# Optimization experiments

Measured on AMD Instinct MI355X. Metric: run time of the kernel, lower is better.

The kernel has to match this reference:

```python
import jax, jax.numpy as jnp
import numpy as np

MARGIN = 1.0
NUM_CLASSES = 128


def setup_inputs() -> dict:
    key = jax.random.key(0)
    k1, k2, k3, k4, k5, k6 = jax.random.split(key, 6)
    B, D, C = 131072, 256, NUM_CLASSES
    return {
        "embeddings": jax.random.normal(k1, (B, D), dtype=jnp.float32),
        "labels": jax.random.randint(k2, (B,), 0, C),
        "W": jax.random.normal(k3, (C, D), dtype=jnp.float32),
        "b": jax.random.normal(k4, (C,), dtype=jnp.float32),
        "r_pos": jax.random.randint(k5, (B,), 0, 1000000007),
        "r_neg": jax.random.randint(k6, (B,), 0, 1000000007),
    }


def reference(embeddings, labels, W, b, r_pos, r_neg):
    B = embeddings.shape[0]
    C = W.shape[0]
    labels = labels.astype(jnp.int32)
    r_pos = r_pos.astype(jnp.int32)
    r_neg = r_neg.astype(jnp.int32)

    # ---- classifier under no_grad: argmax/top-2 of softmax == of logits ----
    logits = jax.lax.stop_gradient(embeddings) @ W.T + b  # [B, C]
    _, top2 = jax.lax.top_k(logits, 2)
    predicted = top2[:, 0]
    runner_up = top2[:, 1]
    correct = predicted == labels
    target_neg = jnp.where(correct, runner_up, predicted)  # [B]

    # ---- per-class segments: sort indices by label once ----
    counts = jnp.zeros((C,), jnp.int32).at[labels].add(1)      # [C]
    starts = jnp.cumsum(counts) - counts                       # [C] segment starts
    order = jnp.argsort(labels).astype(jnp.int32)              # [B] sorted-by-label index list
    inv = jnp.zeros((B,), jnp.int32).at[order].set(jnp.arange(B, dtype=jnp.int32))
    rank = inv - starts[labels]                                # anchor's position within its class segment

    # ---- vectorized masked random sampling ----
    n_pos = counts[labels] - 1                                 # positives exclude the anchor itself
    pr = r_pos % jnp.maximum(n_pos, 1)
    pr = pr + (pr >= rank).astype(jnp.int32)                   # skip over anchor's own slot
    pos_idx = order[starts[labels] + pr]

    n_neg = counts[target_neg]                                 # target_neg != label, anchor never in set
    nr = r_neg % jnp.maximum(n_neg, 1)
    neg_idx = order[starts[target_neg] + nr]

    # ---- triplet margin loss ----
    d_pos = jnp.linalg.norm(embeddings - embeddings[pos_idx], axis=1)
    d_neg = jnp.linalg.norm(embeddings - embeddings[neg_idx], axis=1)
    loss = jnp.maximum(d_pos - d_neg + MARGIN, 0.0)

    valid = (n_pos > 0) & (n_neg > 0)
    loss = loss * valid.astype(loss.dtype)
    denom = jnp.maximum(valid.sum(), 1).astype(loss.dtype)
    return loss.sum() / denom
```

## Files before the change

kernel.cpp:

```cpp
#include <hip/hip_runtime.h>
#include <cstdint>
#include <cstddef>

constexpr int D = 256;
constexpr int C = 128;
constexpr float MARGIN = 1.0f;

typedef __attribute__((ext_vector_type(8))) short short8;
typedef __attribute__((ext_vector_type(4))) float f32x4;

__device__ inline unsigned f2bf(float x) {
    unsigned u = __float_as_uint(x);
    return (u + 0x7FFFu + ((u >> 16) & 1u)) >> 16;
}

__device__ inline void cvt_split8(const float* xs, short8& h, short8& l) {
#pragma unroll
    for (int j = 0; j < 8; ++j) {
        float x = xs[j];
        unsigned hb = f2bf(x);
        h[j] = (short)hb;
        float hf = __uint_as_float(hb << 16);
        l[j] = (short)f2bf(x - hf);
    }
}

__device__ __forceinline__ void merge_top2(float& v1, int& i1, float& v2, int& i2,
                                           float w1, int j1, float w2, int j2)
{
    bool b = (w1 > v1) || (w1 == v1 && j1 < i1);
    float best_v = b ? w1 : v1; int best_i = b ? j1 : i1;
    float lose_v = b ? v1 : w1; int lose_i = b ? i1 : j1;
    float sec_v  = b ? w2 : v2; int sec_i  = b ? j2 : i2;
    bool c = (lose_v > sec_v) || (lose_v == sec_v && lose_i < sec_i);
    v1 = best_v; i1 = best_i;
    v2 = c ? lose_v : sec_v; i2 = c ? lose_i : sec_i;
}

__launch_bounds__(512, 4)
__global__ void k1_logits_top2(const float* __restrict__ emb,
                               const int*   __restrict__ labels,
                               const float* __restrict__ W,
                               const float* __restrict__ bias,
                               int*         __restrict__ target_neg,
                               unsigned short* __restrict__ embh,
                               int do_store)
{
    __shared__ char ldsW[C * 512];
    __shared__ float ldsBias[C];
    const int tid = threadIdx.x;

#pragma unroll
    for (int c = tid; c < 4096; c += 512) {
        int n = c >> 5, slot = c & 31;
        const float* src = W + n * 256 + slot * 8;
        float4 f0 = *(const float4*)src;
        float4 f1 = *(const float4*)(src + 4);
        short8 h;
        h[0] = (short)f2bf(f0.x); h[1] = (short)f2bf(f0.y);
        h[2] = (short)f2bf(f0.z); h[3] = (short)f2bf(f0.w);
        h[4] = (short)f2bf(f1.x); h[5] = (short)f2bf(f1.y);
        h[6] = (short)f2bf(f1.z); h[7] = (short)f2bf(f1.w);
        int dst = (n * 512 + slot * 16) ^ ((n & 7) << 4);
        *(short8*)(ldsW + dst) = h;
    }
    if (tid < C) ldsBias[tid] = bias[tid];
    __syncthreads();

    const int wid = tid >> 6, lane = tid & 63;
    const int l15 = lane & 15, lq = lane >> 4;
    const long row0 = (long)blockIdx.x * 256 + wid * 32;

    f32x4 acc[2][8];
#pragma unroll
    for (int rt = 0; rt < 2; ++rt)
#pragma unroll
        for (int t = 0; t < 8; ++t) acc[rt][t] = (f32x4){0.f, 0.f, 0.f, 0.f};

    const float* e0 = emb + (size_t)(row0 + l15) * D + 8 * lq;
    const float* e1 = e0 + (size_t)16 * D;
    char* eh0 = (char*)embh + (size_t)(row0 + l15) * 512 + 16 * lq;
    char* eh1 = eh0 + (size_t)16 * 512;
    const int xm = (l15 & 7) << 4;

#pragma unroll
    for (int s = 0; s < 8; ++s) {
        float x0[8], x1[8];
        *(float4*)&x0[0] = *(const float4*)(e0 + 32 * s);
        *(float4*)&x0[4] = *(const float4*)(e0 + 32 * s + 4);
        *(float4*)&x1[0] = *(const float4*)(e1 + 32 * s);
        *(float4*)&x1[4] = *(const float4*)(e1 + 32 * s + 4);
        short8 a0h, a0l, a1h, a1l;
        cvt_split8(x0, a0h, a0l);
        cvt_split8(x1, a1h, a1l);
        if (do_store) {
            *(short8*)(eh0 + 64 * s) = a0h;
            *(short8*)(eh1 + 64 * s) = a1h;
        }
#pragma unroll
        for (int t = 0; t < 8; ++t) {
            int addr = ((16 * t + l15) * 512 + 64 * s + 16 * lq) ^ xm;
            short8 bh = *(const short8*)(ldsW + addr);
            acc[0][t] = __builtin_amdgcn_mfma_f32_16x16x32_bf16(a0h, bh, acc[0][t], 0, 0, 0);
            acc[0][t] = __builtin_amdgcn_mfma_f32_16x16x32_bf16(a0l, bh, acc[0][t], 0, 0, 0);
            acc[1][t] = __builtin_amdgcn_mfma_f32_16x16x32_bf16(a1h, bh, acc[1][t], 0, 0, 0);
            acc[1][t] = __builtin_amdgcn_mfma_f32_16x16x32_bf16(a1l, bh, acc[1][t], 0, 0, 0);
        }
    }

    float bv[8];
#pragma unroll
    for (int t = 0; t < 8; ++t) bv[t] = ldsBias[16 * t + l15];

    float v1[8], v2[8]; int i1[8], i2[8];
#pragma unroll
    for (int rt = 0; rt < 2; ++rt)
#pragma unroll
        for (int reg = 0; reg < 4; ++reg) {
            int sIdx = rt * 4 + reg;
            float a1 = -3.4e38f, a2 = -3.4e38f; int c1 = -1, c2 = -1;
#pragma unroll
            for (int t = 0; t < 8; ++t) {
                float v = acc[rt][t][reg] + bv[t];
                int c = 16 * t + l15;
                if (v > a1) { a2 = a1; c2 = c1; a1 = v; c1 = c; }
                else if (v > a2) { a2 = v; c2 = c; }
            }
            v1[sIdx] = a1; i1[sIdx] = c1; v2[sIdx] = a2; i2[sIdx] = c2;
        }
#pragma unroll
    for (int step = 1; step <= 8; step <<= 1) {
#pragma unroll
        for (int sIdx = 0; sIdx < 8; ++sIdx) {
            float w1 = __shfl_xor(v1[sIdx], step);
            int   j1 = __shfl_xor(i1[sIdx], step);
            float w2 = __shfl_xor(v2[sIdx], step);
            int   j2 = __shfl_xor(i2[sIdx], step);
            merge_top2(v1[sIdx], i1[sIdx], v2[sIdx], i2[sIdx], w1, j1, w2, j2);
        }
    }
    if (l15 == 0) {
#pragma unroll
        for (int rt = 0; rt < 2; ++rt)
#pragma unroll
            for (int reg = 0; reg < 4; ++reg) {
                int sIdx = rt * 4 + reg;
                long grow = row0 + rt * 16 + lq * 4 + reg;
                int lab = labels[grow];
                target_neg[grow] = (i1[sIdx] == lab) ? i2[sIdx] : i1[sIdx];
            }
    }
}

__global__ void k2_hist(const int* __restrict__ labels, int* __restrict__ hist, int nchunk)
{
    const int chunk = blockIdx.x * 4 + (threadIdx.x >> 6);
    const int lane = threadIdx.x & 63;
    const int i = chunk * 64 + lane;
    const int lab = labels[i];
    unsigned long long m = ~0ull;
#pragma unroll
    for (int b = 0; b < 7; ++b) {
        unsigned long long bal = __ballot((lab >> b) & 1);
        m &= ((lab >> b) & 1) ? bal : ~bal;
    }
    const int prefix = __popcll(m & ((1ull << lane) - 1ull));
    if (prefix == 0) hist[lab * nchunk + chunk] = __popcll(m);
}

__global__ void k3_scan(int* __restrict__ hist, int* __restrict__ counts, int nchunk)
{
    const int c = blockIdx.x;
    const int tid = threadIdx.x;
    const int per = nchunk / 256;
    const int base = c * nchunk + tid * per;
    int v[8];
    int s = 0;
#pragma unroll
    for (int j = 0; j < 8; ++j) {
        int x = (j < per) ? hist[base + j] : 0;
        v[j] = s; s += x;
    }
    __shared__ int sm[256];
    sm[tid] = s;
    __syncthreads();
    for (int off = 1; off < 256; off <<= 1) {
        int x = (tid >= off) ? sm[tid - off] : 0;
        __syncthreads();
        sm[tid] += x;
        __syncthreads();
    }
    const int excl = sm[tid] - s;
#pragma unroll
    for (int j = 0; j < 8; ++j)
        if (j < per) hist[base + j] = excl + v[j];
    if (tid == 255) counts[c] = sm[255];
}

__global__ void k3b_start(const int* __restrict__ counts, int* __restrict__ class_start)
{
    if (threadIdx.x == 0 && blockIdx.x == 0) {
        int s = 0;
        for (int c = 0; c < C; ++c) { class_start[c] = s; s += counts[c]; }
    }
}

__global__ void k4_scatter(const int* __restrict__ labels, const int* __restrict__ hist,
                           const int* __restrict__ class_start,
                           int* __restrict__ order, int* __restrict__ rankArr, int nchunk)
{
    const int chunk = blockIdx.x * 4 + (threadIdx.x >> 6);
    const int lane = threadIdx.x & 63;
    const int i = chunk * 64 + lane;
    const int lab = labels[i];
    unsigned long long m = ~0ull;
#pragma unroll
    for (int b = 0; b < 7; ++b) {
        unsigned long long bal = __ballot((lab >> b) & 1);
        m &= ((lab >> b) & 1) ? bal : ~bal;
    }
    const int prefix = __popcll(m & ((1ull << lane) - 1ull));
    const int rank = hist[lab * nchunk + chunk] + prefix;
    order[class_start[lab] + rank] = i;
    rankArr[i] = rank;
}

__device__ inline void acc_pair(unsigned a, unsigned b, float& s) {
    float d0 = __uint_as_float(a << 16)        - __uint_as_float(b << 16);
    float d1 = __uint_as_float(a & 0xFFFF0000u) - __uint_as_float(b & 0xFFFF0000u);
    s = fmaf(d0, d0, s);
    s = fmaf(d1, d1, s);
}
__device__ inline void acc16(uint4 a, uint4 b, float& s) {
    acc_pair(a.x, b.x, s); acc_pair(a.y, b.y, s);
    acc_pair(a.z, b.z, s); acc_pair(a.w, b.w, s);
}

__launch_bounds__(256)
__global__ void k56_dist(const unsigned short* __restrict__ embh,
                         const float* __restrict__ embf,
                         const int* __restrict__ labels, const int* __restrict__ target_neg,
                         const int* __restrict__ counts, const int* __restrict__ class_start,
                         const int* __restrict__ order, const int* __restrict__ rankArr,
                         const int* __restrict__ r_pos, const int* __restrict__ r_neg,
                         float* __restrict__ ploss, int* __restrict__ pcnt,
                         int B, int use_bf16)
{
    const int lane = threadIdx.x & 63;
    const int wid = threadIdx.x >> 6;
    const int l16 = threadIdx.x & 15;
    const int g = (blockIdx.x * blockDim.x + threadIdx.x) >> 4;
    const int ngroups = (gridDim.x * blockDim.x) >> 4;
    float lsum = 0.0f;
    int lcnt = 0;
    for (int row = g; row < B; row += ngroups) {
        const int lab = labels[row];
        const int tn = target_neg[row];
        const int n_pos = counts[lab] - 1;
        const int n_neg = counts[tn];
        if (n_pos > 0 && n_neg > 0) {
            int pr = r_pos[row] % n_pos;
            pr += (pr >= rankArr[row]) ? 1 : 0;
            const int p = order[class_start[lab] + pr];
            const int nr = r_neg[row] % n_neg;
            const int n = order[class_start[tn] + nr];
            float dp = 0.0f, dn = 0.0f;
            if (use_bf16) {
                const uint4* a4 = (const uint4*)(embh + (size_t)row * D);
                const uint4* p4 = (const uint4*)(embh + (size_t)p   * D);
                const uint4* n4 = (const uint4*)(embh + (size_t)n   * D);
                uint4 av0 = a4[2 * l16], av1 = a4[2 * l16 + 1];
                uint4 pv0 = p4[2 * l16], pv1 = p4[2 * l16 + 1];
                uint4 nv0 = n4[2 * l16], nv1 = n4[2 * l16 + 1];
                acc16(av0, pv0, dp); acc16(av1, pv1, dp);
                acc16(av0, nv0, dn); acc16(av1, nv1, dn);
            } else {
                const float4* a4 = (const float4*)(embf + (size_t)row * D);
                const float4* p4 = (const float4*)(embf + (size_t)p   * D);
                const float4* n4 = (const float4*)(embf + (size_t)n   * D);
#pragma unroll
                for (int j = 0; j < 4; ++j) {
                    float4 a  = a4[l16 + 16 * j];
                    float4 bp = p4[l16 + 16 * j];
                    float4 bn = n4[l16 + 16 * j];
                    float dx;
                    dx = a.x - bp.x; dp = fmaf(dx, dx, dp);
                    dx = a.y - bp.y; dp = fmaf(dx, dx, dp);
                    dx = a.z - bp.z; dp = fmaf(dx, dx, dp);
                    dx = a.w - bp.w; dp = fmaf(dx, dx, dp);
                    dx = a.x - bn.x; dn = fmaf(dx, dx, dn);
                    dx = a.y - bn.y; dn = fmaf(dx, dx, dn);
                    dx = a.z - bn.z; dn = fmaf(dx, dx, dn);
                    dx = a.w - bn.w; dn = fmaf(dx, dx, dn);
                }
            }
#pragma unroll
            for (int off = 8; off >= 1; off >>= 1) {
                dp += __shfl_xor(dp, off);
                dn += __shfl_xor(dn, off);
            }
            if (l16 == 0) {
                float l = sqrtf(dp) - sqrtf(dn) + MARGIN;
                lsum += fmaxf(l, 0.0f);
                lcnt += 1;
            }
        }
    }
    lsum += __shfl_xor(lsum, 16); lcnt += __shfl_xor(lcnt, 16);
    lsum += __shfl_xor(lsum, 32); lcnt += __shfl_xor(lcnt, 32);
    __shared__ float sl[4];
    __shared__ int   sc[4];
    if (lane == 0) { sl[wid] = lsum; sc[wid] = lcnt; }
    __syncthreads();
    if (threadIdx.x == 0) {
        ploss[blockIdx.x] = sl[0] + sl[1] + sl[2] + sl[3];
        pcnt[blockIdx.x]  = sc[0] + sc[1] + sc[2] + sc[3];
    }
}

__global__ void k6_final(const float* __restrict__ ploss, const int* __restrict__ pcnt,
                         float* __restrict__ out, int nb)
{
    const int tid = threadIdx.x;
    float s = 0.0f; int c = 0;
    for (int j = tid; j < nb; j += 256) { s += ploss[j]; c += pcnt[j]; }
    __shared__ float sf[256];
    __shared__ int   si[256];
    sf[tid] = s; si[tid] = c;
    __syncthreads();
    for (int off = 128; off >= 1; off >>= 1) {
        if (tid < off) { sf[tid] += sf[tid + off]; si[tid] += si[tid + off]; }
        __syncthreads();
    }
    if (tid == 0) out[0] = sf[0] / (float)max(si[0], 1);
}

extern "C" void kernel_launch(void* const* d_in, const int* in_sizes, int n_in,
                              void* d_out, int out_size, void* d_ws, size_t ws_size,
                              hipStream_t stream) {
    const float* emb    = (const float*)d_in[0];
    const int*   labels = (const int*)d_in[1];
    const float* W      = (const float*)d_in[2];
    const float* bias   = (const float*)d_in[3];
    const int*   r_pos  = (const int*)d_in[4];
    const int*   r_neg  = (const int*)d_in[5];
    float* out = (float*)d_out;

    const int B = in_sizes[1];
    const int nchunk = B / 64;
    const int NB5 = 2048;

    size_t off = 0;
    auto alloc = [&](size_t bytes) -> void* {
        void* p = (char*)d_ws + off;
        off += (bytes + 255) & ~(size_t)255;
        return p;
    };
    int* hist        = (int*)alloc((size_t)C * nchunk * 4);
    int* counts      = (int*)alloc(C * 4);
    int* class_start = (int*)alloc(C * 4);
    int* target_neg  = (int*)alloc((size_t)B * 4);
    int* rankArr     = (int*)alloc((size_t)B * 4);
    int* order       = (int*)alloc((size_t)B * 4);
    float* ploss     = (float*)alloc((size_t)NB5 * 4);
    int* pcnt        = (int*)alloc((size_t)NB5 * 4);
    if (off > ws_size) return;

    unsigned short* embh = (unsigned short*)alloc((size_t)B * D * 2);
    const int use_bf16 = (off <= ws_size) ? 1 : 0;

    hipMemsetAsync(hist, 0, (size_t)C * nchunk * 4, stream);

    k1_logits_top2<<<B / 256, 512, 0, stream>>>(emb, labels, W, bias, target_neg,
                                                use_bf16 ? embh : (unsigned short*)target_neg,
                                                use_bf16);
    k2_hist<<<nchunk / 4, 256, 0, stream>>>(labels, hist, nchunk);
    k3_scan<<<C, 256, 0, stream>>>(hist, counts, nchunk);
    k3b_start<<<1, 64, 0, stream>>>(counts, class_start);
    k4_scatter<<<nchunk / 4, 256, 0, stream>>>(labels, hist, class_start, order, rankArr, nchunk);
    k56_dist<<<NB5, 256, 0, stream>>>(embh, emb, labels, target_neg, counts, class_start,
                                      order, rankArr, r_pos, r_neg, ploss, pcnt, B, use_bf16);
    k6_final<<<1, 256, 0, stream>>>(ploss, pcnt, out, NB5);
}
```

Baseline: 286.9 us.

## Transpose histogram layout, parallelize class scan, precompute sample indices, prefetch loads

The histogram is stored chunk-major with every class written per chunk, which removes the memset and gives coalesced writes. The class-start prefix sum now runs as a wave-parallel shuffle scan instead of a single serial thread. Positive and negative sample indices are computed in a separate kernel so the distance kernel only gathers two index arrays and prefetches the next row's indices. The logits kernel also software-pipelines its embedding loads one step ahead. This adds a kernel launch and extra index traffic, and uses more registers.

```diff
diff --git a/kernel.cpp b/kernel.cpp
--- a/kernel.cpp
+++ b/kernel.cpp
@@ -83,13 +83,22 @@
     char* eh1 = eh0 + (size_t)16 * 512;
     const int xm = (l15 & 7) << 4;
 
+    float4 pa0 = *(const float4*)(e0);
+    float4 pa1 = *(const float4*)(e0 + 4);
+    float4 pb0 = *(const float4*)(e1);
+    float4 pb1 = *(const float4*)(e1 + 4);
+
 #pragma unroll
     for (int s = 0; s < 8; ++s) {
         float x0[8], x1[8];
-        *(float4*)&x0[0] = *(const float4*)(e0 + 32 * s);
-        *(float4*)&x0[4] = *(const float4*)(e0 + 32 * s + 4);
-        *(float4*)&x1[0] = *(const float4*)(e1 + 32 * s);
-        *(float4*)&x1[4] = *(const float4*)(e1 + 32 * s + 4);
+        *(float4*)&x0[0] = pa0; *(float4*)&x0[4] = pa1;
+        *(float4*)&x1[0] = pb0; *(float4*)&x1[4] = pb1;
+        if (s < 7) {
+            pa0 = *(const float4*)(e0 + 32 * (s + 1));
+            pa1 = *(const float4*)(e0 + 32 * (s + 1) + 4);
+            pb0 = *(const float4*)(e1 + 32 * (s + 1));
+            pb1 = *(const float4*)(e1 + 32 * (s + 1) + 4);
+        }
         short8 a0h, a0l, a1h, a1l;
         cvt_split8(x0, a0h, a0l);
         cvt_split8(x1, a1h, a1l);
@@ -152,20 +161,22 @@
     }
 }
 
-__global__ void k2_hist(const int* __restrict__ labels, int* __restrict__ hist, int nchunk)
+__global__ void k2_hist(const int* __restrict__ labels, int* __restrict__ hist)
 {
     const int chunk = blockIdx.x * 4 + (threadIdx.x >> 6);
     const int lane = threadIdx.x & 63;
-    const int i = chunk * 64 + lane;
-    const int lab = labels[i];
-    unsigned long long m = ~0ull;
-#pragma unroll
-    for (int b = 0; b < 7; ++b) {
-        unsigned long long bal = __ballot((lab >> b) & 1);
-        m &= ((lab >> b) & 1) ? bal : ~bal;
-    }
-    const int prefix = __popcll(m & ((1ull << lane) - 1ull));
-    if (prefix == 0) hist[lab * nchunk + chunk] = __popcll(m);
+    const int lab = labels[chunk * 64 + lane];
+    unsigned long long bal[7];
+#pragma unroll
+    for (int b = 0; b < 7; ++b) bal[b] = __ballot((lab >> b) & 1);
+#pragma unroll
+    for (int h = 0; h < 2; ++h) {
+        const int c = lane + 64 * h;
+        unsigned long long m = ~0ull;
+#pragma unroll
+        for (int b = 0; b < 7; ++b) m &= ((c >> b) & 1) ? bal[b] : ~bal[b];
+        hist[chunk * C + c] = __popcll(m);
+    }
 }
 
 __global__ void k3_scan(int* __restrict__ hist, int* __restrict__ counts, int nchunk)
@@ -173,12 +184,11 @@
     const int c = blockIdx.x;
     const int tid = threadIdx.x;
     const int per = nchunk / 256;
-    const int base = c * nchunk + tid * per;
     int v[8];
     int s = 0;
 #pragma unroll
     for (int j = 0; j < 8; ++j) {
-        int x = (j < per) ? hist[base + j] : 0;
+        int x = (j < per) ? hist[(tid * per + j) * C + c] : 0;
         v[j] = s; s += x;
     }
     __shared__ int sm[256];
@@ -193,21 +203,29 @@
     const int excl = sm[tid] - s;
 #pragma unroll
     for (int j = 0; j < 8; ++j)
-        if (j < per) hist[base + j] = excl + v[j];
+        if (j < per) hist[(tid * per + j) * C + c] = excl + v[j];
     if (tid == 255) counts[c] = sm[255];
 }
 
 __global__ void k3b_start(const int* __restrict__ counts, int* __restrict__ class_start)
 {
-    if (threadIdx.x == 0 && blockIdx.x == 0) {
-        int s = 0;
-        for (int c = 0; c < C; ++c) { class_start[c] = s; s += counts[c]; }
-    }
+    const int l = threadIdx.x;
+    int c0 = counts[l], c1 = counts[l + 64];
+    int x = c0, y = c1;
+#pragma unroll
+    for (int off = 1; off <= 32; off <<= 1) {
+        int vx = __shfl_up(x, off);
+        int vy = __shfl_up(y, off);
+        if (l >= off) { x += vx; y += vy; }
+    }
+    int tot0 = __shfl(x, 63);
+    class_start[l] = x - c0;
+    class_start[64 + l] = tot0 + y - c1;
 }
 
 __global__ void k4_scatter(const int* __restrict__ labels, const int* __restrict__ hist,
                            const int* __restrict__ class_start,
-                           int* __restrict__ order, int* __restrict__ rankArr, int nchunk)
+                           int* __restrict__ order, int* __restrict__ rankArr)
 {
     const int chunk = blockIdx.x * 4 + (threadIdx.x >> 6);
     const int lane = threadIdx.x & 63;
@@ -220,13 +238,37 @@
         m &= ((lab >> b) & 1) ? bal : ~bal;
     }
     const int prefix = __popcll(m & ((1ull << lane) - 1ull));
-    const int rank = hist[lab * nchunk + chunk] + prefix;
+    const int rank = hist[chunk * C + lab] + prefix;
     order[class_start[lab] + rank] = i;
     rankArr[i] = rank;
 }
 
+__global__ void k5a_sample(const int* __restrict__ labels, const int* __restrict__ target_neg,
+                           const int* __restrict__ counts, const int* __restrict__ class_start,
+                           const int* __restrict__ order, const int* __restrict__ rankArr,
+                           const int* __restrict__ r_pos, const int* __restrict__ r_neg,
+                           int* __restrict__ pos_idx, int* __restrict__ neg_idx, int B)
+{
+    const int i = blockIdx.x * blockDim.x + threadIdx.x;
+    if (i >= B) return;
+    const int lab = labels[i];
+    const int tn = target_neg[i];
+    const int n_pos = counts[lab] - 1;
+    const int n_neg = counts[tn];
+    int pr = r_pos[i] % max(n_pos, 1);
+    pr += (pr >= rankArr[i]) ? 1 : 0;
+    int ppos = class_start[lab] + pr; if (ppos > B - 1) ppos = B - 1;
+    const int pidx = order[ppos];
+    int nr = r_neg[i] % max(n_neg, 1);
+    int npos = class_start[tn] + nr; if (npos > B - 1) npos = B - 1;
+    const int nidx = order[npos];
+    const bool valid = (n_pos > 0) && (n_neg > 0);
+    pos_idx[i] = valid ? pidx : -1;
+    neg_idx[i] = nidx;
+}
+
 __device__ inline void acc_pair(unsigned a, unsigned b, float& s) {
-    float d0 = __uint_as_float(a << 16)        - __uint_as_float(b << 16);
+    float d0 = __uint_as_float(a << 16)         - __uint_as_float(b << 16);
     float d1 = __uint_as_float(a & 0xFFFF0000u) - __uint_as_float(b & 0xFFFF0000u);
     s = fmaf(d0, d0, s);
     s = fmaf(d1, d1, s);
@@ -239,10 +281,7 @@
 __launch_bounds__(256)
 __global__ void k56_dist(const unsigned short* __restrict__ embh,
                          const float* __restrict__ embf,
-                         const int* __restrict__ labels, const int* __restrict__ target_neg,
-                         const int* __restrict__ counts, const int* __restrict__ class_start,
-                         const int* __restrict__ order, const int* __restrict__ rankArr,
-                         const int* __restrict__ r_pos, const int* __restrict__ r_neg,
+                         const int* __restrict__ pos_idx, const int* __restrict__ neg_idx,
                          float* __restrict__ ploss, int* __restrict__ pcnt,
                          int B, int use_bf16)
 {
@@ -253,17 +292,13 @@
     const int ngroups = (gridDim.x * blockDim.x) >> 4;
     float lsum = 0.0f;
     int lcnt = 0;
+    int p_next = (g < B) ? pos_idx[g] : -1;
+    int n_next = (g < B) ? neg_idx[g] : 0;
     for (int row = g; row < B; row += ngroups) {
-        const int lab = labels[row];
-        const int tn = target_neg[row];
-        const int n_pos = counts[lab] - 1;
-        const int n_neg = counts[tn];
-        if (n_pos > 0 && n_neg > 0) {
-            int pr = r_pos[row] % n_pos;
-            pr += (pr >= rankArr[row]) ? 1 : 0;
-            const int p = order[class_start[lab] + pr];
-            const int nr = r_neg[row] % n_neg;
-            const int n = order[class_start[tn] + nr];
+        const int p = p_next, n = n_next;
+        const int nrow = row + ngroups;
+        if (nrow < B) { p_next = pos_idx[nrow]; n_next = neg_idx[nrow]; }
+        if (p >= 0) {
             float dp = 0.0f, dn = 0.0f;
             if (use_bf16) {
                 const uint4* a4 = (const uint4*)(embh + (size_t)row * D);
@@ -362,6 +397,8 @@
     int* target_neg  = (int*)alloc((size_t)B * 4);
     int* rankArr     = (int*)alloc((size_t)B * 4);
     int* order       = (int*)alloc((size_t)B * 4);
+    int* pos_idx     = (int*)alloc((size_t)B * 4);
+    int* neg_idx     = (int*)alloc((size_t)B * 4);
     float* ploss     = (float*)alloc((size_t)NB5 * 4);
     int* pcnt        = (int*)alloc((size_t)NB5 * 4);
     if (off > ws_size) return;
@@ -369,16 +406,16 @@
     unsigned short* embh = (unsigned short*)alloc((size_t)B * D * 2);
     const int use_bf16 = (off <= ws_size) ? 1 : 0;
 
-    hipMemsetAsync(hist, 0, (size_t)C * nchunk * 4, stream);
-
     k1_logits_top2<<<B / 256, 512, 0, stream>>>(emb, labels, W, bias, target_neg,
                                                 use_bf16 ? embh : (unsigned short*)target_neg,
                                                 use_bf16);
-    k2_hist<<<nchunk / 4, 256, 0, stream>>>(labels, hist, nchunk);
+    k2_hist<<<nchunk / 4, 256, 0, stream>>>(labels, hist);
     k3_scan<<<C, 256, 0, stream>>>(hist, counts, nchunk);
     k3b_start<<<1, 64, 0, stream>>>(counts, class_start);
-    k4_scatter<<<nchunk / 4, 256, 0, stream>>>(labels, hist, class_start, order, rankArr, nchunk);
-    k56_dist<<<NB5, 256, 0, stream>>>(embh, emb, labels, target_neg, counts, class_start,
-                                      order, rankArr, r_pos, r_neg, ploss, pcnt, B, use_bf16);
+    k4_scatter<<<nchunk / 4, 256, 0, stream>>>(labels, hist, class_start, order, rankArr);
+    k5a_sample<<<(B + 255) / 256, 256, 0, stream>>>(labels, target_neg, counts, class_start,
+                                                    order, rankArr, r_pos, r_neg,
+                                                    pos_idx, neg_idx, B);
+    k56_dist<<<NB5, 256, 0, stream>>>(embh, emb, pos_idx, neg_idx, ploss, pcnt, B, use_bf16);
     k6_final<<<1, 256, 0, stream>>>(ploss, pcnt, out, NB5);
 }
```

New measurement: 292.0 us. About the same (+1.8%).
